# Performance work log

Hardware: AMD Instinct MI355X
Metric: run time of the kernel (lower is better)

## Reference

```python
import jax, jax.numpy as jnp
import numpy as np

B, C, H, W = 8, 384, 32, 32
NH, DK, DV = 8, 48, 48
CFF = 4 * C
L = H * W
NBIAS = (2 * H - 1) * (2 * W - 1)
LN_EPS = 1e-5


def _relative_indices(height, width):
    # rel_idx[q, k] = (gy_k - gy_q + H) * W + (gx_k - gx_q + W), matching the torch loop
    gy, gx = np.meshgrid(np.arange(height), np.arange(width), indexing='ij')
    gy = gy.ravel(); gx = gx.ravel()
    rel = (gy[None, :] - gy[:, None] + height) * width + (gx[None, :] - gx[:, None] + width)
    return jnp.asarray(rel, dtype=jnp.int64)


def setup_inputs() -> dict:
    key = jax.random.key(0)
    ks = jax.random.split(key, 10)
    s = 0.02  # small init scale
    return {
        'x': jax.random.normal(ks[0], (B, C, H, W), dtype=jnp.float32),
        'gamma': jnp.ones((C,), jnp.float32),
        'beta': jnp.zeros((C,), jnp.float32),
        'Wq': jax.random.normal(ks[1], (NH * DK, C), jnp.float32) * s,
        'Wk': jax.random.normal(ks[2], (NH * DK, C), jnp.float32) * s,
        'Wv': jax.random.normal(ks[3], (NH * DV, C), jnp.float32) * s,
        'Wo': jax.random.normal(ks[4], (C, NH * DV), jnp.float32) * s,
        'bo': jnp.zeros((C,), jnp.float32),
        'rel_bias': jax.random.normal(ks[5], (NH, NBIAS), jnp.float32),
        'fc1_w': jax.random.normal(ks[6], (CFF, C), jnp.float32) * s,
        'fc1_b': jnp.zeros((CFF,), jnp.float32),
        'fc2_w': jax.random.normal(ks[7], (C, CFF), jnp.float32) * s,
        'fc2_b': jnp.zeros((C,), jnp.float32),
        'rel_idx': _relative_indices(H, W),
    }


def reference(x, gamma, beta, Wq, Wk, Wv, Wo, bo, rel_bias,
              fc1_w, fc1_b, fc2_w, fc2_b, rel_idx):
    b, c, h_sp, w_sp = x.shape
    l = h_sp * w_sp
    nh = rel_bias.shape[0]
    dk = Wq.shape[0] // nh
    dv = Wv.shape[0] // nh

    # LayerNorm over channel dim (NHWC), then flatten to tokens [b, l, c]
    t = jnp.transpose(x, (0, 2, 3, 1))
    mu = jnp.mean(t, axis=-1, keepdims=True)
    var = jnp.mean(jnp.square(t - mu), axis=-1, keepdims=True)
    t = (t - mu) / jnp.sqrt(var + LN_EPS) * gamma + beta
    tok = t.reshape(b, l, c)

    q = (tok @ Wq.T).reshape(b, l, nh, dk)
    k = (tok @ Wk.T).reshape(b, l, nh, dk)
    v = (tok @ Wv.T).reshape(b, l, nh, dv)

    # gathered relative position bias: [nh, l, l]
    bias = rel_bias[:, rel_idx]
    # note: original applies NO 1/sqrt(d_k) scaling
    scores = jnp.einsum('blhd,bmhd->bhlm', q, k) + bias[None]
    attn = jax.nn.softmax(scores, axis=-1)
    out = jnp.einsum('bhlm,bmhd->blhd', attn, v).reshape(b, l, nh * dv)
    out = out @ Wo.T + bo  # [b, l, c]
    out = jnp.transpose(out, (0, 2, 1)).reshape(b, c, h_sp, w_sp)

    y = x + out  # attention residual (x_stem = x, no downsampling)

    # FFN: 1x1 convs == per-pixel linear over channels; exact (erf) gelu as torch default
    u = jnp.einsum('bchw,oc->bohw', y, fc1_w) + fc1_b[None, :, None, None]
    u = jax.nn.gelu(u, approximate=False)
    u = jnp.einsum('bchw,oc->bohw', u, fc2_w) + fc2_b[None, :, None, None]
    return y + u
```

## Files before the change

### kernel.cpp

```cpp
#include <hip/hip_runtime.h>
#include <math.h>

#define SL 1024
#define CH 384
#define NHEAD 8
#define DH 48
#define NBIAS 3969
#define NTOK 8192
#define BATCH 8
#define CFF 1536
#define LN_EPS 1e-5f
#define QKVLD 1152

#define WQKV_OFF 0
#define WO_OFF   442368
#define F1_OFF   589824
#define F2_OFF   1179648
#define WTOT     1769472

typedef float floatx4 __attribute__((ext_vector_type(4)));
typedef short bf16x8 __attribute__((ext_vector_type(8)));

__device__ __forceinline__ unsigned f2bf_u(float f) {
  unsigned u = __float_as_uint(f);
  return (u + 0x7fffu + ((u >> 16) & 1u)) >> 16;
}
__device__ __forceinline__ unsigned pack2(float a, float b) {
  return f2bf_u(a) | (f2bf_u(b) << 16);
}

__device__ __forceinline__ void gload_lds16(const void* g, void* l) {
  __builtin_amdgcn_global_load_lds(
      (const __attribute__((address_space(1))) void*)g,
      (__attribute__((address_space(3))) void*)l, 16, 0, 0);
}

__global__ void k_w2bf(const float* __restrict__ Wq, const float* __restrict__ Wk,
                       const float* __restrict__ Wv, const float* __restrict__ Wo,
                       const float* __restrict__ f1, const float* __restrict__ f2,
                       short* __restrict__ dst) {
  size_t i = ((size_t)blockIdx.x * 256 + threadIdx.x) * 8;
  if (i >= WTOT) return;
  const float* s;
  size_t base;
  if (i < 147456)        { s = Wq; base = 0; }
  else if (i < 294912)   { s = Wk; base = 147456; }
  else if (i < WO_OFF)   { s = Wv; base = 294912; }
  else if (i < F1_OFF)   { s = Wo; base = WO_OFF; }
  else if (i < F2_OFF)   { s = f1; base = F1_OFF; }
  else                   { s = f2; base = F2_OFF; }
  const float4* p = (const float4*)(s + (i - base));
  float4 a = p[0], b = p[1];
  uint4 o;
  o.x = pack2(a.x, a.y); o.y = pack2(a.z, a.w);
  o.z = pack2(b.x, b.y); o.w = pack2(b.z, b.w);
  *(uint4*)(dst + i) = o;
}

__global__ __launch_bounds__(256) void k_ln_fused(
    const float* __restrict__ x, const float* __restrict__ gamma,
    const float* __restrict__ beta, short* __restrict__ tok) {
  __shared__ float sx[32][385];
  int b = blockIdx.y, l0 = blockIdx.x * 32;
  int tid = threadIdx.x;
  const float* xb = x + (size_t)b * CH * SL;
  int cr = tid >> 3, ls = (tid & 7) * 4;
#pragma unroll
  for (int c0 = 0; c0 < CH; c0 += 32) {
    int c = c0 + cr;
    float4 v = *(const float4*)(xb + (size_t)c * SL + l0 + ls);
    sx[ls + 0][c] = v.x; sx[ls + 1][c] = v.y;
    sx[ls + 2][c] = v.z; sx[ls + 3][c] = v.w;
  }
  __syncthreads();
  int tl = tid >> 3, p = tid & 7;
  float vals[48];
  float s = 0.f, q = 0.f;
#pragma unroll
  for (int i = 0; i < 48; i++) {
    float v = sx[tl][p * 48 + i];
    vals[i] = v; s += v; q += v * v;
  }
  s += __shfl_xor(s, 1, 64); q += __shfl_xor(q, 1, 64);
  s += __shfl_xor(s, 2, 64); q += __shfl_xor(q, 2, 64);
  s += __shfl_xor(s, 4, 64); q += __shfl_xor(q, 4, 64);
  float mu = s * (1.0f / CH);
  float rstd = rsqrtf(q * (1.0f / CH) - mu * mu + LN_EPS);
  short* orow = tok + (size_t)(b * SL + l0 + tl) * CH + p * 48;
#pragma unroll
  for (int i = 0; i < 48; i += 2) {
    float a = (vals[i] - mu) * rstd * gamma[p * 48 + i] + beta[p * 48 + i];
    float c = (vals[i + 1] - mu) * rstd * gamma[p * 48 + i + 1] + beta[p * 48 + i + 1];
    *(unsigned*)(orow + i) = pack2(a, c);
  }
}

template <int BM, bool GELU, bool HAS_BIAS, int RES_MODE, int OUT_MODE>
__global__ __launch_bounds__(256) void k_gemm_mfma(
    const short* __restrict__ A, const short* __restrict__ W,
    const float* __restrict__ bias, const float* __restrict__ res,
    float* __restrict__ Cf, short* __restrict__ Cb, float* __restrict__ Ct,
    int N, int K) {
  constexpr int MI = BM / 32;
  constexpr int ASI = BM * 2 / 64;
  __shared__ short As[BM * 64];
  __shared__ short Bs[128 * 64];
  int tid = threadIdx.x;
  int wid = tid >> 6, lane = tid & 63;
  int lanelo = lane & 15, quad = lane >> 4;
  int wm = wid & 1, wn = wid >> 1;
  int m0 = blockIdx.y * BM, n0 = blockIdx.x * 128;

  const short* Aga[ASI];
  short* Ala[ASI];
#pragma unroll
  for (int s = 0; s < ASI; s++) {
    int p = wid * (BM * 2) + s * 64 + lane;
    int row = p >> 3, ch = (p & 7) ^ (row & 7);
    Aga[s] = A + (size_t)(m0 + row) * K + ch * 8;
    Ala[s] = As + (wid * (BM * 2) + s * 64) * 8;
  }
  const short* Bga[4];
  short* Bla[4];
#pragma unroll
  for (int s = 0; s < 4; s++) {
    int p = wid * 256 + s * 64 + lane;
    int row = p >> 3, ch = (p & 7) ^ (row & 7);
    Bga[s] = W + (size_t)(n0 + row) * K + ch * 8;
    Bla[s] = Bs + (wid * 256 + s * 64) * 8;
  }

  floatx4 acc[MI][4];
#pragma unroll
  for (int i = 0; i < MI; i++)
#pragma unroll
    for (int j = 0; j < 4; j++) acc[i][j] = {0.f, 0.f, 0.f, 0.f};

  int x8 = lanelo & 7;
  int ca0 = (quad ^ x8) * 8;
  int ca1 = ((quad + 4) ^ x8) * 8;

  for (int k0 = 0; k0 < K; k0 += 64) {
    __syncthreads();
#pragma unroll
    for (int s = 0; s < ASI; s++) gload_lds16(Aga[s] + k0, Ala[s]);
#pragma unroll
    for (int s = 0; s < 4; s++) gload_lds16(Bga[s] + k0, Bla[s]);
    __syncthreads();
#pragma unroll
    for (int h = 0; h < 2; h++) {
      int co = h ? ca1 : ca0;
      bf16x8 af[MI], bq[4];
#pragma unroll
      for (int i = 0; i < MI; i++)
        af[i] = *(const bf16x8*)&As[(wm * (BM / 2) + i * 16 + lanelo) * 64 + co];
#pragma unroll
      for (int j = 0; j < 4; j++)
        bq[j] = *(const bf16x8*)&Bs[(wn * 64 + j * 16 + lanelo) * 64 + co];
#pragma unroll
      for (int i = 0; i < MI; i++)
#pragma unroll
        for (int j = 0; j < 4; j++)
          acc[i][j] = __builtin_amdgcn_mfma_f32_16x16x32_bf16(af[i], bq[j], acc[i][j], 0, 0, 0);
    }
  }

  int colb = n0 + wn * 64 + lanelo;
  float bvv[4];
#pragma unroll
  for (int j = 0; j < 4; j++) bvv[j] = HAS_BIAS ? bias[colb + j * 16] : 0.0f;
#pragma unroll
  for (int i = 0; i < MI; i++) {
    int r = m0 + wm * (BM / 2) + i * 16 + quad * 4;
    int bb = r >> 10, ll = r & 1023;
#pragma unroll
    for (int j = 0; j < 4; j++) {
      int c = colb + j * 16;
      float4 rv = {0.f, 0.f, 0.f, 0.f};
      if (RES_MODE == 2) rv = *(const float4*)(res + ((size_t)bb * CH + c) * SL + ll);
      float vv[4];
#pragma unroll
      for (int reg = 0; reg < 4; reg++) {
        float v = acc[i][j][reg] + bvv[j];
        if (RES_MODE == 1) v += res[(size_t)(r + reg) * N + c];
        if (RES_MODE == 2) v += (&rv.x)[reg];
        if (GELU) v = 0.5f * v * (1.0f + erff(v * 0.7071067811865476f));
        vv[reg] = v;
      }
      if (OUT_MODE & 1) {
#pragma unroll
        for (int reg = 0; reg < 4; reg++) Cf[(size_t)(r + reg) * N + c] = vv[reg];
      }
      if (OUT_MODE & 2) {
#pragma unroll
        for (int reg = 0; reg < 4; reg++) Cb[(size_t)(r + reg) * N + c] = (short)f2bf_u(vv[reg]);
      }
      if (OUT_MODE & 4) {
        float4 ov = {vv[0], vv[1], vv[2], vv[3]};
        *(float4*)(Ct + ((size_t)bb * CH + c) * SL + ll) = ov;
      }
    }
  }
}

__global__ __launch_bounds__(256) void k_attn_mfma(
    const short* __restrict__ qkv, const float* __restrict__ rel_bias,
    short* __restrict__ ao) {
  __shared__ short QP[128 * 72];
  __shared__ short Ks[64 * 72];
  __shared__ short Vts[48 * 72];

  int b = blockIdx.z, h = blockIdx.y;
  int l0 = blockIdx.x * 128;
  int tid = threadIdx.x;
  int wid = tid >> 6, lane = tid & 63;
  int lanelo = lane & 15, quad = lane >> 4;
  size_t bSL = (size_t)b * SL;
  const float* rbh = rel_bias + h * NBIAS;

  int srow = tid / 3, spos = tid - srow * 3;
  int vmp = tid & 31, vdg = tid >> 5;

  for (int g = tid; g < 768; g += 256) {
    int row = g / 6, pos = g - row * 6;
    *(uint4*)&QP[row * 72 + pos * 8] =
        *(const uint4*)(qkv + (bSL + l0 + row) * QKVLD + h * DH + pos * 8);
  }
  for (int z = tid; z < 128 * 8; z += 256) {
    int r = z >> 3, u = z & 7;
    ((unsigned*)&QP[r * 72 + 48])[u] = 0u;
    if (r < 64) ((unsigned*)&Ks[r * 72 + 48])[u] = 0u;
  }
  __syncthreads();

  bf16x8 aq[2][2];
#pragma unroll
  for (int i = 0; i < 2; i++) {
    aq[i][0] = *(const bf16x8*)&QP[(wid * 32 + i * 16 + lanelo) * 72 + quad * 8];
    aq[i][1] = *(const bf16x8*)&QP[(wid * 32 + i * 16 + lanelo) * 72 + 32 + quad * 8];
  }

  floatx4 O[2][3];
#pragma unroll
  for (int i = 0; i < 2; i++)
#pragma unroll
    for (int d = 0; d < 3; d++) O[i][d] = {0.f, 0.f, 0.f, 0.f};
  float lsum[2][4] = {{0.f, 0.f, 0.f, 0.f}, {0.f, 0.f, 0.f, 0.f}};
  int boff[2];
#pragma unroll
  for (int i = 0; i < 2; i++)
    boff[i] = 1056 - (l0 + wid * 32 + i * 16 + quad * 4) + lanelo;

  short* Pw = &QP[wid * 32 * 72];

  for (int mt = 0; mt < SL; mt += 64) {
    __syncthreads();
    if (tid < 192) {
      {
        const short* src = qkv + (bSL + mt + srow) * QKVLD + 384 + h * DH;
        *(uint4*)&Ks[srow * 72 + spos * 8]      = *(const uint4*)(src + spos * 8);
        *(uint4*)&Ks[srow * 72 + 24 + spos * 8] = *(const uint4*)(src + 24 + spos * 8);
      }
      {
        const short* vs0 = qkv + (bSL + mt + 2 * vmp) * QKVLD + 768 + h * DH + vdg * 8;
        union { uint4 u; unsigned short s[8]; } va, vb;
        va.u = *(const uint4*)vs0;
        vb.u = *(const uint4*)(vs0 + QKVLD);
#pragma unroll
        for (int i = 0; i < 8; i++) {
          unsigned pk = (unsigned)va.s[i] | ((unsigned)vb.s[i] << 16);
          *(unsigned*)&Vts[(vdg * 8 + i) * 72 + 2 * vmp] = pk;
        }
      }
    }
    __syncthreads();

    bf16x8 kb[4][2];
#pragma unroll
    for (int nt = 0; nt < 4; nt++) {
      kb[nt][0] = *(const bf16x8*)&Ks[(nt * 16 + lanelo) * 72 + quad * 8];
      kb[nt][1] = *(const bf16x8*)&Ks[(nt * 16 + lanelo) * 72 + 32 + quad * 8];
    }

#pragma unroll
    for (int i = 0; i < 2; i++) {
      floatx4 s[4];
#pragma unroll
      for (int nt = 0; nt < 4; nt++) {
        floatx4 a = {0.f, 0.f, 0.f, 0.f};
        a = __builtin_amdgcn_mfma_f32_16x16x32_bf16(aq[i][0], kb[nt][0], a, 0, 0, 0);
        a = __builtin_amdgcn_mfma_f32_16x16x32_bf16(aq[i][1], kb[nt][1], a, 0, 0, 0);
        s[nt] = a;
      }
#pragma unroll
      for (int nt = 0; nt < 4; nt++) {
        int mo = mt + nt * 16;
#pragma unroll
        for (int reg = 0; reg < 4; reg++) {
          float e = __expf(s[nt][reg] + rbh[boff[i] - reg + mo]);
          lsum[i][reg] += e;
          Pw[(i * 16 + quad * 4 + reg) * 72 + nt * 16 + lanelo] = (short)f2bf_u(e);
        }
      }
    }
    __asm__ volatile("s_waitcnt lgkmcnt(0)" ::: "memory");
    bf16x8 pa[2][2];
#pragma unroll
    for (int i = 0; i < 2; i++) {
      pa[i][0] = *(const bf16x8*)&Pw[(i * 16 + lanelo) * 72 + quad * 8];
      pa[i][1] = *(const bf16x8*)&Pw[(i * 16 + lanelo) * 72 + 32 + quad * 8];
    }
#pragma unroll
    for (int d = 0; d < 3; d++) {
      bf16x8 v0 = *(const bf16x8*)&Vts[(d * 16 + lanelo) * 72 + quad * 8];
      bf16x8 v1 = *(const bf16x8*)&Vts[(d * 16 + lanelo) * 72 + 32 + quad * 8];
#pragma unroll
      for (int i = 0; i < 2; i++) {
        O[i][d] = __builtin_amdgcn_mfma_f32_16x16x32_bf16(pa[i][0], v0, O[i][d], 0, 0, 0);
        O[i][d] = __builtin_amdgcn_mfma_f32_16x16x32_bf16(pa[i][1], v1, O[i][d], 0, 0, 0);
      }
    }
  }

#pragma unroll
  for (int i = 0; i < 2; i++)
#pragma unroll
    for (int reg = 0; reg < 4; reg++) {
      float s = lsum[i][reg];
      s += __shfl_xor(s, 1, 64);
      s += __shfl_xor(s, 2, 64);
      s += __shfl_xor(s, 4, 64);
      s += __shfl_xor(s, 8, 64);
      float inv = 1.0f / s;
      size_t base =
          (bSL + (size_t)(l0 + wid * 32 + i * 16 + quad * 4 + reg)) * CH + h * DH;
      ao[base + 0 + lanelo]  = (short)f2bf_u(O[i][0][reg] * inv);
      ao[base + 16 + lanelo] = (short)f2bf_u(O[i][1][reg] * inv);
      ao[base + 32 + lanelo] = (short)f2bf_u(O[i][2][reg] * inv);
    }
}

extern "C" void kernel_launch(void* const* d_in, const int* in_sizes, int n_in,
                              void* d_out, int out_size, void* d_ws, size_t ws_size,
                              hipStream_t stream) {
  const float* x = (const float*)d_in[0];
  const float* gamma = (const float*)d_in[1];
  const float* beta = (const float*)d_in[2];
  const float* Wq = (const float*)d_in[3];
  const float* Wk = (const float*)d_in[4];
  const float* Wv = (const float*)d_in[5];
  const float* Wo = (const float*)d_in[6];
  const float* bo = (const float*)d_in[7];
  const float* rel_bias = (const float*)d_in[8];
  const float* fc1_w = (const float*)d_in[9];
  const float* fc1_b = (const float*)d_in[10];
  const float* fc2_w = (const float*)d_in[11];
  const float* fc2_b = (const float*)d_in[12];
  float* out = (float*)d_out;

  const size_t TOKCH = (size_t)NTOK * CH;
  float* ws_f = (float*)d_ws;
  float* yb = ws_f;
  short* wbf    = (short*)(yb + TOKCH);
  short* tok_bf = wbf + WTOT;
  short* qkv_bf = tok_bf + TOKCH;
  short* ao_bf  = qkv_bf + (size_t)NTOK * QKVLD;
  short* yb_bf  = ao_bf + TOKCH;
  short* h1_bf  = yb_bf + TOKCH;

  k_w2bf<<<WTOT / 8 / 256, 256, 0, stream>>>(Wq, Wk, Wv, Wo, fc1_w, fc2_w, wbf);
  k_ln_fused<<<dim3(SL / 32, BATCH), 256, 0, stream>>>(x, gamma, beta, tok_bf);

  k_gemm_mfma<128, false, false, 0, 2>
      <<<dim3(QKVLD / 128, NTOK / 128), 256, 0, stream>>>(
          tok_bf, wbf + WQKV_OFF, nullptr, nullptr, nullptr, qkv_bf, nullptr,
          QKVLD, CH);

  k_attn_mfma<<<dim3(SL / 128, NHEAD, BATCH), 256, 0, stream>>>(qkv_bf, rel_bias, ao_bf);

  k_gemm_mfma<64, false, true, 2, 3>
      <<<dim3(CH / 128, NTOK / 64), 256, 0, stream>>>(
          ao_bf, wbf + WO_OFF, bo, x, yb, yb_bf, nullptr, CH, CH);

  k_gemm_mfma<128, true, true, 0, 2>
      <<<dim3(CFF / 128, NTOK / 128), 256, 0, stream>>>(
          yb_bf, wbf + F1_OFF, fc1_b, nullptr, nullptr, h1_bf, nullptr, CFF, CH);

  k_gemm_mfma<64, false, true, 1, 4>
      <<<dim3(CH / 128, NTOK / 64), 256, 0, stream>>>(
          h1_bf, wbf + F2_OFF, fc2_b, yb, nullptr, nullptr, out, CH, CFF);
}
```

Before: 218.5 us.

## Store QKV head-major and register-prefetch next K/V tile in attention

The QKV projection GEMM now writes its output in a head-major layout [3][B*NH][L][48], so each attention block reads K, V and Q as contiguous per-head slabs instead of rows strided by 1152 elements. The attention loop also loads the next K/V tile into registers right after the shared-memory barrier, overlapping global loads with the MFMA compute of the current tile. The cost is more scattered 2-byte stores in the GEMM epilogue and extra register pressure in the attention kernel.

After: 224.4 us. 1.03x slower.

```diff
diff --git a/kernel.cpp b/kernel.cpp
--- a/kernel.cpp
+++ b/kernel.cpp
@@ -11,6 +11,7 @@
 #define CFF 1536
 #define LN_EPS 1e-5f
 #define QKVLD 1152
+#define HMS 3145728
 
 #define WQKV_OFF 0
 #define WO_OFF   442368
@@ -100,7 +101,7 @@
     const short* __restrict__ A, const short* __restrict__ W,
     const float* __restrict__ bias, const float* __restrict__ res,
     float* __restrict__ Cf, short* __restrict__ Cb, float* __restrict__ Ct,
-    int N, int K) {
+    short* __restrict__ Chm, int N, int K) {
   constexpr int MI = BM / 32;
   constexpr int ASI = BM * 2 / 64;
   __shared__ short As[BM * 64];
@@ -199,12 +200,22 @@
         float4 ov = {vv[0], vv[1], vv[2], vv[3]};
         *(float4*)(Ct + ((size_t)bb * CH + c) * SL + ll) = ov;
       }
+      if (OUT_MODE & 8) {
+        int part = c / 384;
+        int rem = c - part * 384;
+        int hh = rem / 48, dd = rem - hh * 48;
+        short* dst = Chm + (size_t)part * HMS +
+                     ((size_t)(bb * NHEAD + hh) * SL + ll) * 48 + dd;
+#pragma unroll
+        for (int reg = 0; reg < 4; reg++) dst[reg * 48] = (short)f2bf_u(vv[reg]);
+      }
     }
   }
 }
 
 __global__ __launch_bounds__(256) void k_attn_mfma(
-    const short* __restrict__ qkv, const float* __restrict__ rel_bias,
+    const short* __restrict__ qh, const short* __restrict__ kh,
+    const short* __restrict__ vh, const float* __restrict__ rel_bias,
     short* __restrict__ ao) {
   __shared__ short QP[128 * 72];
   __shared__ short Ks[64 * 72];
@@ -215,22 +226,37 @@
   int tid = threadIdx.x;
   int wid = tid >> 6, lane = tid & 63;
   int lanelo = lane & 15, quad = lane >> 4;
+  size_t hb = ((size_t)b * NHEAD + h) * SL;
   size_t bSL = (size_t)b * SL;
   const float* rbh = rel_bias + h * NBIAS;
-
-  int srow = tid / 3, spos = tid - srow * 3;
-  int vmp = tid & 31, vdg = tid >> 5;
-
-  for (int g = tid; g < 768; g += 256) {
-    int row = g / 6, pos = g - row * 6;
-    *(uint4*)&QP[row * 72 + pos * 8] =
-        *(const uint4*)(qkv + (bSL + l0 + row) * QKVLD + h * DH + pos * 8);
+  const short* kbase = kh + hb * 48;
+  const short* vbase = vh + hb * 48;
+
+  {
+    const short* qsrc = qh + (hb + l0) * 48;
+    for (int g = tid; g < 768; g += 256) {
+      int row = g / 6, pos = g - row * 6;
+      *(uint4*)&QP[row * 72 + pos * 8] = *(const uint4*)(qsrc + g * 8);
+    }
   }
   for (int z = tid; z < 128 * 8; z += 256) {
     int r = z >> 3, u = z & 7;
     ((unsigned*)&QP[r * 72 + 48])[u] = 0u;
     if (r < 64) ((unsigned*)&Ks[r * 72 + 48])[u] = 0u;
   }
+
+  int kg = 2 * tid;
+  int krow = kg / 6, kpos = kg - krow * 6;
+  int vmp = tid & 31, vdg = tid >> 5;
+
+  uint4 kr0, kr1, vr0, vr1;
+  if (tid < 192) {
+    kr0 = *(const uint4*)(kbase + kg * 8);
+    kr1 = *(const uint4*)(kbase + kg * 8 + 8);
+    const short* vs = vbase + (2 * vmp) * 48 + vdg * 8;
+    vr0 = *(const uint4*)vs;
+    vr1 = *(const uint4*)(vs + 48);
+  }
   __syncthreads();
 
   bf16x8 aq[2][2];
@@ -256,24 +282,25 @@
   for (int mt = 0; mt < SL; mt += 64) {
     __syncthreads();
     if (tid < 192) {
-      {
-        const short* src = qkv + (bSL + mt + srow) * QKVLD + 384 + h * DH;
-        *(uint4*)&Ks[srow * 72 + spos * 8]      = *(const uint4*)(src + spos * 8);
-        *(uint4*)&Ks[srow * 72 + 24 + spos * 8] = *(const uint4*)(src + 24 + spos * 8);
-      }
-      {
-        const short* vs0 = qkv + (bSL + mt + 2 * vmp) * QKVLD + 768 + h * DH + vdg * 8;
-        union { uint4 u; unsigned short s[8]; } va, vb;
-        va.u = *(const uint4*)vs0;
-        vb.u = *(const uint4*)(vs0 + QKVLD);
-#pragma unroll
-        for (int i = 0; i < 8; i++) {
-          unsigned pk = (unsigned)va.s[i] | ((unsigned)vb.s[i] << 16);
-          *(unsigned*)&Vts[(vdg * 8 + i) * 72 + 2 * vmp] = pk;
-        }
+      *(uint4*)&Ks[krow * 72 + kpos * 8] = kr0;
+      *(uint4*)&Ks[krow * 72 + (kpos + 1) * 8] = kr1;
+      union { uint4 u; unsigned short s[8]; } va, vb;
+      va.u = vr0; vb.u = vr1;
+#pragma unroll
+      for (int i = 0; i < 8; i++) {
+        unsigned pk = (unsigned)va.s[i] | ((unsigned)vb.s[i] << 16);
+        *(unsigned*)&Vts[(vdg * 8 + i) * 72 + 2 * vmp] = pk;
       }
     }
     __syncthreads();
+    if (mt + 64 < SL && tid < 192) {
+      const short* ks = kbase + (size_t)(mt + 64) * 48;
+      kr0 = *(const uint4*)(ks + kg * 8);
+      kr1 = *(const uint4*)(ks + kg * 8 + 8);
+      const short* vs = vbase + (size_t)(mt + 64 + 2 * vmp) * 48 + vdg * 8;
+      vr0 = *(const uint4*)vs;
+      vr1 = *(const uint4*)(vs + 48);
+    }
 
     bf16x8 kb[4][2];
 #pragma unroll
@@ -363,30 +390,32 @@
   float* yb = ws_f;
   short* wbf    = (short*)(yb + TOKCH);
   short* tok_bf = wbf + WTOT;
-  short* qkv_bf = tok_bf + TOKCH;
-  short* ao_bf  = qkv_bf + (size_t)NTOK * QKVLD;
+  short* hm     = tok_bf + TOKCH;
+  short* ao_bf  = hm + 3 * (size_t)HMS;
   short* yb_bf  = ao_bf + TOKCH;
   short* h1_bf  = yb_bf + TOKCH;
 
   k_w2bf<<<WTOT / 8 / 256, 256, 0, stream>>>(Wq, Wk, Wv, Wo, fc1_w, fc2_w, wbf);
   k_ln_fused<<<dim3(SL / 32, BATCH), 256, 0, stream>>>(x, gamma, beta, tok_bf);
 
-  k_gemm_mfma<128, false, false, 0, 2>
+  k_gemm_mfma<128, false, false, 0, 8>
       <<<dim3(QKVLD / 128, NTOK / 128), 256, 0, stream>>>(
-          tok_bf, wbf + WQKV_OFF, nullptr, nullptr, nullptr, qkv_bf, nullptr,
-          QKVLD, CH);
-
-  k_attn_mfma<<<dim3(SL / 128, NHEAD, BATCH), 256, 0, stream>>>(qkv_bf, rel_bias, ao_bf);
+          tok_bf, wbf + WQKV_OFF, nullptr, nullptr, nullptr, nullptr, nullptr,
+          hm, QKVLD, CH);
+
+  k_attn_mfma<<<dim3(SL / 128, NHEAD, BATCH), 256, 0, stream>>>(
+      hm, hm + HMS, hm + 2 * (size_t)HMS, rel_bias, ao_bf);
 
   k_gemm_mfma<64, false, true, 2, 3>
       <<<dim3(CH / 128, NTOK / 64), 256, 0, stream>>>(
-          ao_bf, wbf + WO_OFF, bo, x, yb, yb_bf, nullptr, CH, CH);
+          ao_bf, wbf + WO_OFF, bo, x, yb, yb_bf, nullptr, nullptr, CH, CH);
 
   k_gemm_mfma<128, true, true, 0, 2>
       <<<dim3(CFF / 128, NTOK / 128), 256, 0, stream>>>(
-          yb_bf, wbf + F1_OFF, fc1_b, nullptr, nullptr, h1_bf, nullptr, CFF, CH);
+          yb_bf, wbf + F1_OFF, fc1_b, nullptr, nullptr, h1_bf, nullptr, nullptr,
+          CFF, CH);
 
   k_gemm_mfma<64, false, true, 1, 4>
       <<<dim3(CH / 128, NTOK / 64), 256, 0, stream>>>(
-          h1_bf, wbf + F2_OFF, fc2_b, yb, nullptr, nullptr, out, CH, CFF);
-}
+          h1_bf, wbf + F2_OFF, fc2_b, yb, nullptr, nullptr, out, nullptr, CH, CFF);
+}
```
